# Performance work log

Measured on AMD Instinct MI355X. Metric: run time of the kernel, lower is better.

The kernel has to match this reference:

```python
import jax, jax.numpy as jnp
import numpy as np
from jax import lax

# NLM hyperparameters (from init_kwargs)
H_PARAM = 7.0 / 255.0          # OpenCV h is in 0-255 intensity units; images are in [0,1]
H2 = H_PARAM * H_PARAM
T = 7                          # template (patch) window size
TH = T // 2
S = 21                         # search window size
SH = S // 2


def setup_inputs() -> dict:
    key = jax.random.key(0)
    x = jax.random.uniform(key, (4, 1, 1024, 1024), dtype=jnp.float32)
    return {"x": x}


def _box_mean(d):
    # mean filter over TxT template window with reflect ('same') padding,
    # done as two separable 1D convolutions.
    k = (jnp.ones((T,), dtype=d.dtype) / T)
    dp = jnp.pad(d, ((0, 0), (0, 0), (TH, TH), (TH, TH)), mode="reflect")
    dn = ("NCHW", "OIHW", "NCHW")
    y = lax.conv_general_dilated(dp, k.reshape(1, 1, T, 1), (1, 1), "VALID", dimension_numbers=dn)
    y = lax.conv_general_dilated(y, k.reshape(1, 1, 1, T), (1, 1), "VALID", dimension_numbers=dn)
    return y


def reference(x):
    B, C, H, W = x.shape
    xc = jnp.clip(x, 0.0, 1.0)
    # reflect-pad by the search radius so every shift is a plain slice
    padded = jnp.pad(xc, ((0, 0), (0, 0), (SH, SH), (SH, SH)), mode="reflect")

    # all SxS = 441 search-window offsets, as padded-array slice origins in [0, 2*SH]
    oy, ox = jnp.meshgrid(jnp.arange(S, dtype=jnp.int32), jnp.arange(S, dtype=jnp.int32), indexing="ij")
    offsets = jnp.stack([oy.reshape(-1), ox.reshape(-1)], axis=-1)  # [441, 2]

    zero = jnp.int32(0)

    def body(carry, off):
        wsum, vsum = carry
        shifted = lax.dynamic_slice(padded, (zero, zero, off[0], off[1]), (B, C, H, W))
        dist = _box_mean((xc - shifted) ** 2)          # mean squared patch difference
        w = jnp.exp(-dist / H2)                        # NLM similarity weight
        return (wsum + w, vsum + w * shifted), None

    init = (jnp.zeros_like(xc), jnp.zeros_like(xc))
    (wsum, vsum), _ = lax.scan(body, init, offsets)
    out = vsum / wsum
    return jnp.clip(out, 0.0, 1.0)
```

## Files before the change

### kernel.cpp

```cpp
#include <hip/hip_runtime.h>
#include <cstddef>


constexpr int TS    = 32;
constexpr int XSTR  = 61;
constexpr int XROWS = 59;
constexpr int XSZ   = XROWS * XSTR;
constexpr int VSTR  = 42;
constexpr int VROWS = 33;
constexpr int VS_SZ = VROWS * VSTR;
constexpr int NBUF  = 4;

__device__ __forceinline__ int refl(int i, int n) {
    i = (i < 0) ? -i : i;
    return (i >= n) ? (2 * n - 2 - i) : i;
}

template<bool FAST>
__device__ __forceinline__ void nlm_body(const float* __restrict__ img,
                                         float* __restrict__ out,
                                         int H, int W, int gx0, int gy0,
                                         float* __restrict__ xs,
                                         float* __restrict__ vsh, int tid)
{
    for (int e = tid; e < XSZ; e += 256) {
        int i = e / XSTR, j = e - i * XSTR;
        int jj = (j > 57) ? 57 : j;
        int gy = refl(gy0 - 13 + i, H);
        int gx = refl(gx0 - 13 + jj, W);
        float v = img[(size_t)gy * W + gx];
        xs[e] = fminf(fmaxf(v, 0.0f), 1.0f);
    }
    __syncthreads();

    const bool bv = (tid < 114);
    float u[17];
    int   aB = 0;
    int   aS[17];
    int   wb = 0;
    {
        int t  = bv ? tid : 0;
        int g  = t / 38;
        int cc = t - g * 38;
        int r  = g * 11;
        int mxm10 = refl(gx0 + cc - 3, W) - gx0 + 3;
        if constexpr (FAST) {
            aB = r * XSTR + mxm10;
#pragma unroll
            for (int i = 0; i < 17; ++i)
                u[i] = xs[(r + i + 10) * XSTR + mxm10 + 10];
        } else {
#pragma unroll
            for (int i = 0; i < 17; ++i) {
                int my = refl(gy0 + r + i - 3, H) - gy0 + 13;
                u[i]  = xs[my * XSTR + mxm10 + 10];
                aS[i] = (my - 10) * XSTR + mxm10;
            }
        }
        wb = r * VSTR + cc;
    }

    const bool cact = (tid >= 128);
    const int ct = cact ? (tid - 128) : 0;
    const int py = ct >> 2;
    const int c8 = (ct & 3) * 8;
    const int vb = py * VSTR + c8;
    int svC = (py + 3) * XSTR + (c8 + 3);

    int oxB = 0;
    int oxC = 0;

    float p[7];
    float ws[8], ac[8];
#pragma unroll
    for (int k = 0; k < 8; ++k) { ws[k] = 0.f; ac[k] = 0.f; }
    const float K = -(65025.0f / 2401.0f) * 1.4426950408889634f;

    auto bv_step = [&](int buf) {
        if (bv) {
            float* vo = vsh + buf * VS_SZ + wb;
            float q[17];
            if constexpr (FAST) {
#pragma unroll
                for (int i = 0; i < 17; ++i)
                    q[i] = xs[aB + i * XSTR];
            } else {
#pragma unroll
                for (int i = 0; i < 17; ++i)
                    q[i] = xs[aS[i]];
            }
#pragma unroll
            for (int i = 0; i < 17; ++i) {
                float d = u[i] - q[i];
                q[i] = d * d;
            }
            float s[11];
            s[0] = ((q[0] + q[1]) + (q[2] + q[3])) + ((q[4] + q[5]) + q[6]);
#pragma unroll
            for (int k = 1; k < 11; ++k)
                s[k] = s[k - 1] + (q[k + 6] - q[k - 1]);
#pragma unroll
            for (int k = 0; k < 11; ++k)
                vo[k * VSTR] = s[k];
            if constexpr (FAST) {
                aB += (oxB == 20) ? (XSTR - 20) : 1;
            } else {
                int step = (oxB == 20) ? (XSTR - 20) : 1;
#pragma unroll
                for (int i = 0; i < 17; ++i) aS[i] += step;
            }
        }
        oxB = (oxB == 20) ? 0 : (oxB + 1);
    };

    auto c_step = [&](int buf) {
        if (cact) {
            if (oxC == 0) {
#pragma unroll
                for (int k = 0; k < 7; ++k) p[k] = xs[svC + k];
            }
            const float2* vp =
                reinterpret_cast<const float2*>(vsh + buf * VS_SZ + vb);
            float2 tA = vp[0], tB = vp[1], tC = vp[2], tD = vp[3];
            float2 tE = vp[4], tF = vp[5], tG = vp[6];
            float p7 = xs[svC + 7 + oxC];
            float h0 = ((tA.x + tA.y) + (tB.x + tB.y)) + ((tC.x + tC.y) + tD.x);
            float h1 = h0 - tA.x + tD.y;
            float h2 = h1 - tA.y + tE.x;
            float h3 = h2 - tB.x + tE.y;
            float h4 = h3 - tB.y + tF.x;
            float h5 = h4 - tC.x + tF.y;
            float h6 = h5 - tC.y + tG.x;
            float h7 = h6 - tD.x + tG.y;
            float w;
            w = __builtin_amdgcn_exp2f(h0 * K); ws[0] += w; ac[0] = fmaf(w, p[0], ac[0]);
            w = __builtin_amdgcn_exp2f(h1 * K); ws[1] += w; ac[1] = fmaf(w, p[1], ac[1]);
            w = __builtin_amdgcn_exp2f(h2 * K); ws[2] += w; ac[2] = fmaf(w, p[2], ac[2]);
            w = __builtin_amdgcn_exp2f(h3 * K); ws[3] += w; ac[3] = fmaf(w, p[3], ac[3]);
            w = __builtin_amdgcn_exp2f(h4 * K); ws[4] += w; ac[4] = fmaf(w, p[4], ac[4]);
            w = __builtin_amdgcn_exp2f(h5 * K); ws[5] += w; ac[5] = fmaf(w, p[5], ac[5]);
            w = __builtin_amdgcn_exp2f(h6 * K); ws[6] += w; ac[6] = fmaf(w, p[6], ac[6]);
            w = __builtin_amdgcn_exp2f(h7 * K); ws[7] += w; ac[7] = fmaf(w, p7,   ac[7]);
#pragma unroll
            for (int k = 0; k < 6; ++k) p[k] = p[k + 1];
            p[6] = p7;
        }
        if (oxC == 20) { oxC = 0; svC += XSTR; } else { ++oxC; }
    };

    bv_step(0);
    bv_step(1);
    __syncthreads();
#pragma unroll 1
    for (int i = 2; i < 440; i += 2) {
        bv_step(i & 3);
        bv_step((i + 1) & 3);
        c_step((i - 2) & 3);
        c_step((i - 1) & 3);
        __syncthreads();
    }
    bv_step(0);
    c_step(2);
    c_step(3);
    __syncthreads();
    c_step(0);

    if (cact) {
        float4 oA, oB;
        oA.x = fminf(fmaxf(ac[0] * __builtin_amdgcn_rcpf(ws[0]), 0.f), 1.f);
        oA.y = fminf(fmaxf(ac[1] * __builtin_amdgcn_rcpf(ws[1]), 0.f), 1.f);
        oA.z = fminf(fmaxf(ac[2] * __builtin_amdgcn_rcpf(ws[2]), 0.f), 1.f);
        oA.w = fminf(fmaxf(ac[3] * __builtin_amdgcn_rcpf(ws[3]), 0.f), 1.f);
        oB.x = fminf(fmaxf(ac[4] * __builtin_amdgcn_rcpf(ws[4]), 0.f), 1.f);
        oB.y = fminf(fmaxf(ac[5] * __builtin_amdgcn_rcpf(ws[5]), 0.f), 1.f);
        oB.z = fminf(fmaxf(ac[6] * __builtin_amdgcn_rcpf(ws[6]), 0.f), 1.f);
        oB.w = fminf(fmaxf(ac[7] * __builtin_amdgcn_rcpf(ws[7]), 0.f), 1.f);
        float* op = &out[((size_t)blockIdx.z * H + (gy0 + py)) * W + (gx0 + c8)];
        *reinterpret_cast<float4*>(op)     = oA;
        *reinterpret_cast<float4*>(op + 4) = oB;
    }
}

__global__ __launch_bounds__(256)
void nlm_kernel(const float* __restrict__ img_all, float* __restrict__ out,
                int H, int W) {
    __shared__ __align__(16) float xs[XSZ];
    __shared__ __align__(16) float vsh[NBUF * VS_SZ];
    const int tid = threadIdx.x;
    const int gx0 = blockIdx.x * TS;
    const int gy0 = blockIdx.y * TS;
    const float* img = img_all + (size_t)blockIdx.z * H * W;
    if (gy0 - 3 >= 0 && gy0 + 35 < H)
        nlm_body<true>(img, out, H, W, gx0, gy0, xs, vsh, tid);
    else
        nlm_body<false>(img, out, H, W, gx0, gy0, xs, vsh, tid);
}

extern "C" void kernel_launch(void* const* d_in, const int* in_sizes, int n_in,
                              void* d_out, int out_size, void* d_ws, size_t ws_size,
                              hipStream_t stream) {
    const float* x = (const float*)d_in[0];
    float* out = (float*)d_out;
    const int H = 1024, W = 1024;
    const int B = in_sizes[0] / (H * W);
    dim3 grid(W / TS, H / TS, B);
    nlm_kernel<<<grid, dim3(256), 0, stream>>>(x, out, H, W);
}
```

Before: 972.0 us.

## Skip exp/accumulate when all patch weights underflow; switch to double-buffered distance stage

The weighting stage now takes the minimum of the eight box-summed patch distances per thread. It skips the exp2 and accumulation whenever no lane in the wavefront has a distance at or below a threshold where the weight would underflow to zero. When the work does run, centre pixel values are read from shared memory instead of being kept in a sliding register window. The distance buffer ring is cut from four to two slots, so the loop now processes one offset per barrier instead of two, which doubles the number of barriers. How much is skipped depends on the data: on noise-like inputs many offsets can be skipped, but the ballot adds a branch, and the extra barriers may eat into the savings.

```diff
diff --git a/kernel.cpp b/kernel.cpp
--- a/kernel.cpp
+++ b/kernel.cpp
@@ -9,7 +9,6 @@
 constexpr int VSTR  = 42;
 constexpr int VROWS = 33;
 constexpr int VS_SZ = VROWS * VSTR;
-constexpr int NBUF  = 4;
 
 __device__ __forceinline__ int refl(int i, int n) {
     i = (i < 0) ? -i : i;
@@ -70,11 +69,11 @@
     int oxB = 0;
     int oxC = 0;
 
-    float p[7];
     float ws[8], ac[8];
 #pragma unroll
     for (int k = 0; k < 8; ++k) { ws[k] = 0.f; ac[k] = 0.f; }
     const float K = -(65025.0f / 2401.0f) * 1.4426950408889634f;
+    const float HSKIP = 3.95f;
 
     auto bv_step = [&](int buf) {
         if (bv) {
@@ -115,15 +114,10 @@
 
     auto c_step = [&](int buf) {
         if (cact) {
-            if (oxC == 0) {
-#pragma unroll
-                for (int k = 0; k < 7; ++k) p[k] = xs[svC + k];
-            }
             const float2* vp =
                 reinterpret_cast<const float2*>(vsh + buf * VS_SZ + vb);
             float2 tA = vp[0], tB = vp[1], tC = vp[2], tD = vp[3];
             float2 tE = vp[4], tF = vp[5], tG = vp[6];
-            float p7 = xs[svC + 7 + oxC];
             float h0 = ((tA.x + tA.y) + (tB.x + tB.y)) + ((tC.x + tC.y) + tD.x);
             float h1 = h0 - tA.x + tD.y;
             float h2 = h1 - tA.y + tE.x;
@@ -132,37 +126,36 @@
             float h5 = h4 - tC.x + tF.y;
             float h6 = h5 - tC.y + tG.x;
             float h7 = h6 - tD.x + tG.y;
-            float w;
-            w = __builtin_amdgcn_exp2f(h0 * K); ws[0] += w; ac[0] = fmaf(w, p[0], ac[0]);
-            w = __builtin_amdgcn_exp2f(h1 * K); ws[1] += w; ac[1] = fmaf(w, p[1], ac[1]);
-            w = __builtin_amdgcn_exp2f(h2 * K); ws[2] += w; ac[2] = fmaf(w, p[2], ac[2]);
-            w = __builtin_amdgcn_exp2f(h3 * K); ws[3] += w; ac[3] = fmaf(w, p[3], ac[3]);
-            w = __builtin_amdgcn_exp2f(h4 * K); ws[4] += w; ac[4] = fmaf(w, p[4], ac[4]);
-            w = __builtin_amdgcn_exp2f(h5 * K); ws[5] += w; ac[5] = fmaf(w, p[5], ac[5]);
-            w = __builtin_amdgcn_exp2f(h6 * K); ws[6] += w; ac[6] = fmaf(w, p[6], ac[6]);
-            w = __builtin_amdgcn_exp2f(h7 * K); ws[7] += w; ac[7] = fmaf(w, p7,   ac[7]);
-#pragma unroll
-            for (int k = 0; k < 6; ++k) p[k] = p[k + 1];
-            p[6] = p7;
+            float m = fminf(fminf(fminf(h0, h1), fminf(h2, h3)),
+                            fminf(fminf(h4, h5), fminf(h6, h7)));
+            if (__builtin_expect(__ballot(m <= HSKIP) != 0ull, 0)) {
+                const int sp = svC + oxC;
+                float x0 = xs[sp],     x1 = xs[sp + 1];
+                float x2 = xs[sp + 2], x3 = xs[sp + 3];
+                float x4 = xs[sp + 4], x5 = xs[sp + 5];
+                float x6 = xs[sp + 6], x7 = xs[sp + 7];
+                float w;
+                w = __builtin_amdgcn_exp2f(h0 * K); ws[0] += w; ac[0] = fmaf(w, x0, ac[0]);
+                w = __builtin_amdgcn_exp2f(h1 * K); ws[1] += w; ac[1] = fmaf(w, x1, ac[1]);
+                w = __builtin_amdgcn_exp2f(h2 * K); ws[2] += w; ac[2] = fmaf(w, x2, ac[2]);
+                w = __builtin_amdgcn_exp2f(h3 * K); ws[3] += w; ac[3] = fmaf(w, x3, ac[3]);
+                w = __builtin_amdgcn_exp2f(h4 * K); ws[4] += w; ac[4] = fmaf(w, x4, ac[4]);
+                w = __builtin_amdgcn_exp2f(h5 * K); ws[5] += w; ac[5] = fmaf(w, x5, ac[5]);
+                w = __builtin_amdgcn_exp2f(h6 * K); ws[6] += w; ac[6] = fmaf(w, x6, ac[6]);
+                w = __builtin_amdgcn_exp2f(h7 * K); ws[7] += w; ac[7] = fmaf(w, x7, ac[7]);
+            }
         }
         if (oxC == 20) { oxC = 0; svC += XSTR; } else { ++oxC; }
     };
 
     bv_step(0);
-    bv_step(1);
     __syncthreads();
 #pragma unroll 1
-    for (int i = 2; i < 440; i += 2) {
-        bv_step(i & 3);
-        bv_step((i + 1) & 3);
-        c_step((i - 2) & 3);
-        c_step((i - 1) & 3);
+    for (int i = 1; i < 441; ++i) {
+        bv_step(i & 1);
+        c_step(1 - (i & 1));
         __syncthreads();
     }
-    bv_step(0);
-    c_step(2);
-    c_step(3);
-    __syncthreads();
     c_step(0);
 
     if (cact) {
@@ -185,7 +178,7 @@
 void nlm_kernel(const float* __restrict__ img_all, float* __restrict__ out,
                 int H, int W) {
     __shared__ __align__(16) float xs[XSZ];
-    __shared__ __align__(16) float vsh[NBUF * VS_SZ];
+    __shared__ __align__(16) float vsh[2 * VS_SZ];
     const int tid = threadIdx.x;
     const int gx0 = blockIdx.x * TS;
     const int gy0 = blockIdx.y * TS;
```

Result: faster. 875.7 us (-9.9%).
